# Kernel tuning notes

Hardware: AMD Instinct MI355X
Metric: run time of the kernel (lower is better)

The kernel has to match this reference:

```python
import jax, jax.numpy as jnp
import numpy as np

EPS = 1e-8  # matches torch F.cosine_similarity eps


def _normalize(x):
    n = jnp.sqrt(jnp.sum(x * x, axis=-1, keepdims=True))
    return x / jnp.maximum(n, EPS)


def _cross_entropy_diag(logits):
    # targets = arange(B): CE = mean(-log_softmax(logits)[i, i])
    logp = jax.nn.log_softmax(logits, axis=-1)
    return -jnp.mean(jnp.diagonal(logp))


def setup_inputs() -> dict:
    key = jax.random.key(0)
    k1, k2, k3 = jax.random.split(key, 3)
    B, D = 8192, 256
    return {
        "heavy_feat": jax.random.normal(k1, (B, D), dtype=jnp.float32),
        "light_feat": jax.random.normal(k2, (B, D), dtype=jnp.float32),
        "antigen_feat": jax.random.normal(k3, (B, D), dtype=jnp.float32),
    }


def reference(heavy_feat, light_feat, antigen_feat):
    h = _normalize(heavy_feat)   # [B, D]
    l = _normalize(light_feat)   # [B, D]
    a = _normalize(antigen_feat)  # [B, D]
    ha_sim = jnp.einsum("id,jd->ij", h, a)  # [B, B] cosine sims
    hl_sim = jnp.einsum("id,jd->ij", l, a)  # [B, B]
    return _cross_entropy_diag(ha_sim) + _cross_entropy_diag(hl_sim)
```

## Files before the change

### kernel.cpp

```cpp
#include <hip/hip_runtime.h>
#include <stdint.h>

#define BN_ 8192
#define DK_ 256
#define LOG2E 1.4426950408889634f
#define INVQ (1.0f / 16129.0f)
#define KQ   (LOG2E / 16129.0f)

typedef __attribute__((ext_vector_type(4))) float f32x4;
typedef __attribute__((ext_vector_type(4))) int i32x4;

#define GLD16(gp, lp)                                                   \
  __builtin_amdgcn_global_load_lds(                                     \
      (__attribute__((address_space(1))) void*)(gp),                    \
      (__attribute__((address_space(3))) void*)(lp), 16, 0, 0)

#define BAR() __builtin_amdgcn_s_barrier()
#define VM4() asm volatile("s_waitcnt vmcnt(4)" ::: "memory")
#define VM0() asm volatile("s_waitcnt vmcnt(0)" ::: "memory")

__global__ __launch_bounds__(256) void norm_kernel(
    const float* __restrict__ hf, const float* __restrict__ lf,
    const float* __restrict__ af, unsigned char* __restrict__ qbase,
    float* __restrict__ sumexp) {
  const int tid = threadIdx.x;
  if (blockIdx.x < 16) {
    f32x4 z = {0.f, 0.f, 0.f, 0.f};
    *(f32x4*)(sumexp + blockIdx.x * 1024 + tid * 4) = z;
  }
  const int w = tid >> 6, lane = tid & 63;
  const int grow = blockIdx.x * 4 + w;
  const int m = grow >> 13;
  const int r = grow & (BN_ - 1);
  const float* src = (m == 0) ? hf : (m == 1) ? lf : af;
  unsigned char* dst = qbase + (size_t)m * BN_ * DK_;
  const float4 v = ((const float4*)(src + (size_t)r * DK_))[lane];
  float ss = v.x * v.x + v.y * v.y + v.z * v.z + v.w * v.w;
#pragma unroll
  for (int mk = 32; mk >= 1; mk >>= 1) ss += __shfl_xor(ss, mk, 64);
  const float inv = 127.0f / fmaxf(sqrtf(ss), 1e-8f);
  const int q0 = (int)rintf(v.x * inv), q1 = (int)rintf(v.y * inv);
  const int q2 = (int)rintf(v.z * inv), q3 = (int)rintf(v.w * inv);
  const unsigned pk = (q0 & 255) | ((q1 & 255) << 8) | ((q2 & 255) << 16) |
                      ((unsigned)(q3 & 255) << 24);
  *(unsigned*)(dst + (size_t)r * DK_ + lane * 4) = pk;
}

__global__ __launch_bounds__(512, 2) void gemm_lse_kernel(
    const unsigned char* __restrict__ hl, const unsigned char* __restrict__ an,
    float* __restrict__ sumexp , float* __restrict__ diag ) {
  extern __shared__ char lds[];

  const int tid = threadIdx.x;
  const int lane = tid & 63, w = tid >> 6;
  const int wr = w >> 2, wc = w & 3;
  const int lmod = lane & 15, lhalf = lane >> 4;

  const int bid = blockIdx.x;
  const int swz = (bid & 7) * 32 + (bid >> 3);
  const int mt = swz >> 1;
  const int cg = swz & 1;

  const int aswz = 16 * ((tid & 15) ^ ((tid >> 4) & 15));
  const unsigned char* aG = hl + (size_t)(mt * 128 + (tid >> 4)) * DK_ + aswz;
  char* aD = lds + tid * 16;
  GLD16(aG, aD);
  GLD16(aG + 8192, aD + 8192);
  GLD16(aG + 16384, aD + 16384);
  GLD16(aG + 24576, aD + 24576);

  const int slog16 = 16 * ((lane & 3) ^ ((lane >> 3) & 3));
  const unsigned char* bB =
      an + (size_t)(cg * 4096 + wc * 64 + (lane >> 2)) * DK_ + slog16;
  char* ldsB = lds + 32768 + w * 8192 + lane * 16;

#define STAGEB(uu)                                                       \
  do {                                                                   \
    const int ct_ = (uu) >> 2, ku_ = (uu) & 3;                           \
    const unsigned char* g_ = bB + ct_ * 65536 + ku_ * 64;               \
    char* d_ = ldsB + ((uu) & 1) * 4096;                                 \
    GLD16(g_, d_);                                                       \
    GLD16(g_ + 4096, d_ + 1024);                                         \
    GLD16(g_ + 8192, d_ + 2048);                                         \
    GLD16(g_ + 12288, d_ + 3072);                                        \
  } while (0)

  STAGEB(0);
  VM4();
  BAR();

  i32x4 afr[4][4];
  {
    const char* aR = lds + (wr * 64 + lmod) * 256;
#pragma unroll
    for (int ku = 0; ku < 4; ++ku)
#pragma unroll
      for (int m = 0; m < 4; ++m)
        afr[ku][m] = *(const i32x4*)(aR + m * 4096 + 16 * ((ku * 4 + lhalf) ^ lmod));
  }

  const int rdoffB = lmod * 64 + 16 * (lhalf ^ ((lmod >> 1) & 3));
  const char* ldsBr = lds + 32768 + w * 8192;

  const int p = mt >> 6;
  const int D = (mt & 63) * 128 + wr * 64;
  const bool dWave = (wc == ((D >> 6) & 3)) && ((D >> 12) == cg);
  const int ctD = (D >> 8) & 15;

  float rsum[4][4];
#pragma unroll
  for (int m = 0; m < 4; ++m)
#pragma unroll
    for (int r = 0; r < 4; ++r) rsum[m][r] = 0.0f;

#pragma unroll 1
  for (int ct = 0; ct < 16; ++ct) {
    i32x4 acc[4][4];
#pragma unroll
    for (int m = 0; m < 4; ++m)
#pragma unroll
      for (int n = 0; n < 4; ++n) acc[m][n] = i32x4{0, 0, 0, 0};

#pragma unroll
    for (int ku = 0; ku < 4; ++ku) {
      const int u = ct * 4 + ku;
      if (u < 63) {
        STAGEB(u + 1);
        VM4();
      } else {
        VM0();
      }
      const char* Lb = ldsBr + (u & 1) * 4096;
      i32x4 bf[4];
#pragma unroll
      for (int n = 0; n < 4; ++n) bf[n] = *(const i32x4*)(Lb + n * 1024 + rdoffB);
#pragma unroll
      for (int m = 0; m < 4; ++m)
#pragma unroll
        for (int n = 0; n < 4; ++n)
          acc[m][n] = __builtin_amdgcn_mfma_i32_16x16x64_i8(afr[ku][m], bf[n], acc[m][n], 0, 0, 0);
    }

    if (dWave && ct == ctD) {
#pragma unroll
      for (int m = 0; m < 4; ++m)
#pragma unroll
        for (int r = 0; r < 4; ++r)
          if (lmod == lhalf * 4 + r)
            diag[p * BN_ + D + m * 16 + lmod] = (float)acc[m][m][r] * INVQ;
    }
#pragma unroll
    for (int m = 0; m < 4; ++m)
#pragma unroll
      for (int n = 0; n < 4; ++n)
#pragma unroll
        for (int r = 0; r < 4; ++r)
          rsum[m][r] += __builtin_amdgcn_exp2f((float)acc[m][n][r] * KQ);
  }

#pragma unroll
  for (int m = 0; m < 4; ++m)
#pragma unroll
    for (int r = 0; r < 4; ++r) {
      float v = rsum[m][r];
      v += __shfl_xor(v, 1, 64);
      v += __shfl_xor(v, 2, 64);
      v += __shfl_xor(v, 4, 64);
      v += __shfl_xor(v, 8, 64);
      if (lmod == 0)
        atomicAdd(&sumexp[p * BN_ + D + m * 16 + lhalf * 4 + r], v);
    }
#undef STAGEB
}

__global__ __launch_bounds__(1024) void finalize_kernel(
    const float* __restrict__ sumexp, const float* __restrict__ diag,
    float* __restrict__ out) {
  const int tid = threadIdx.x;
  float s = 0.0f;
  for (int i = tid; i < 2 * BN_; i += 1024) s += logf(sumexp[i]) - diag[i];
#pragma unroll
  for (int mk = 32; mk >= 1; mk >>= 1) s += __shfl_xor(s, mk, 64);
  __shared__ float red[16];
  if ((tid & 63) == 0) red[tid >> 6] = s;
  __syncthreads();
  if (tid == 0) {
    float t = 0.f;
#pragma unroll
    for (int j = 0; j < 16; ++j) t += red[j];
    out[0] = t * (1.0f / (float)BN_);
  }
}

extern "C" void kernel_launch(void* const* d_in, const int* in_sizes, int n_in,
                              void* d_out, int out_size, void* d_ws, size_t ws_size,
                              hipStream_t stream) {
  const float* hf = (const float*)d_in[0];
  const float* lf = (const float*)d_in[1];
  const float* af = (const float*)d_in[2];

  char* ws = (char*)d_ws;
  const size_t nmat = (size_t)BN_ * DK_;
  unsigned char* qbase = (unsigned char*)ws;
  unsigned char* hl = qbase;
  unsigned char* an = qbase + 2 * nmat;
  float* sumexp = (float*)(ws + 3 * nmat);
  float* diag = sumexp + 2 * BN_;

  hipFuncSetAttribute((const void*)gemm_lse_kernel,
                      hipFuncAttributeMaxDynamicSharedMemorySize, 98304);

  norm_kernel<<<(3 * BN_) / 4, 256, 0, stream>>>(hf, lf, af, qbase, sumexp);
  gemm_lse_kernel<<<256, 512, 98304, stream>>>(hl, an, sumexp, diag);
  finalize_kernel<<<1, 1024, 0, stream>>>(sumexp, diag, (float*)d_out);
}
```

Baseline: 65.09 us.

## Load B fragments directly from global memory and read A fragments from LDS per step

Drops the double-buffered global-to-LDS staging of the antigen (B) tiles and instead loads B fragments straight from global memory into registers in each k-step. A fragments are no longer kept in registers for the whole kernel but re-read from LDS each iteration, and LDS use falls from 96 KB to 32 KB. The aim is to cut register pressure, LDS traffic and the per-step waits and barriers, at the cost of uncoalesced, unpipelined global loads with latency that is exposed, unless occupancy and the L2 hide it.

After: 87.29 us. 1.34x slower.

```diff
diff --git a/kernel.cpp b/kernel.cpp
--- a/kernel.cpp
+++ b/kernel.cpp
@@ -16,7 +16,6 @@
       (__attribute__((address_space(3))) void*)(lp), 16, 0, 0)
 
 #define BAR() __builtin_amdgcn_s_barrier()
-#define VM4() asm volatile("s_waitcnt vmcnt(4)" ::: "memory")
 #define VM0() asm volatile("s_waitcnt vmcnt(0)" ::: "memory")
 
 __global__ __launch_bounds__(256) void norm_kernel(
@@ -68,39 +67,13 @@
   GLD16(aG + 8192, aD + 8192);
   GLD16(aG + 16384, aD + 16384);
   GLD16(aG + 24576, aD + 24576);
-
-  const int slog16 = 16 * ((lane & 3) ^ ((lane >> 3) & 3));
-  const unsigned char* bB =
-      an + (size_t)(cg * 4096 + wc * 64 + (lane >> 2)) * DK_ + slog16;
-  char* ldsB = lds + 32768 + w * 8192 + lane * 16;
-
-#define STAGEB(uu)                                                       \
-  do {                                                                   \
-    const int ct_ = (uu) >> 2, ku_ = (uu) & 3;                           \
-    const unsigned char* g_ = bB + ct_ * 65536 + ku_ * 64;               \
-    char* d_ = ldsB + ((uu) & 1) * 4096;                                 \
-    GLD16(g_, d_);                                                       \
-    GLD16(g_ + 4096, d_ + 1024);                                         \
-    GLD16(g_ + 8192, d_ + 2048);                                         \
-    GLD16(g_ + 12288, d_ + 3072);                                        \
-  } while (0)
-
-  STAGEB(0);
-  VM4();
+  VM0();
   BAR();
 
-  i32x4 afr[4][4];
-  {
-    const char* aR = lds + (wr * 64 + lmod) * 256;
-#pragma unroll
-    for (int ku = 0; ku < 4; ++ku)
-#pragma unroll
-      for (int m = 0; m < 4; ++m)
-        afr[ku][m] = *(const i32x4*)(aR + m * 4096 + 16 * ((ku * 4 + lhalf) ^ lmod));
-  }
+  const char* aR = lds + (wr * 64 + lmod) * 256;
 
-  const int rdoffB = lmod * 64 + 16 * (lhalf ^ ((lmod >> 1) & 3));
-  const char* ldsBr = lds + 32768 + w * 8192;
+  const unsigned char* bG =
+      an + (size_t)(cg * 4096 + wc * 64 + lmod) * DK_ + lhalf * 16;
 
   const int p = mt >> 6;
   const int D = (mt & 63) * 128 + wr * 64;
@@ -121,24 +94,21 @@
 #pragma unroll
       for (int n = 0; n < 4; ++n) acc[m][n] = i32x4{0, 0, 0, 0};
 
+    const unsigned char* bCt = bG + (size_t)ct * 65536;
 #pragma unroll
     for (int ku = 0; ku < 4; ++ku) {
-      const int u = ct * 4 + ku;
-      if (u < 63) {
-        STAGEB(u + 1);
-        VM4();
-      } else {
-        VM0();
-      }
-      const char* Lb = ldsBr + (u & 1) * 4096;
-      i32x4 bf[4];
+      i32x4 af[4], bf[4];
 #pragma unroll
-      for (int n = 0; n < 4; ++n) bf[n] = *(const i32x4*)(Lb + n * 1024 + rdoffB);
+      for (int n = 0; n < 4; ++n)
+        bf[n] = *(const i32x4*)(bCt + n * 4096 + ku * 64);
+#pragma unroll
+      for (int m = 0; m < 4; ++m)
+        af[m] = *(const i32x4*)(aR + m * 4096 + 16 * ((ku * 4 + lhalf) ^ lmod));
 #pragma unroll
       for (int m = 0; m < 4; ++m)
 #pragma unroll
         for (int n = 0; n < 4; ++n)
-          acc[m][n] = __builtin_amdgcn_mfma_i32_16x16x64_i8(afr[ku][m], bf[n], acc[m][n], 0, 0, 0);
+          acc[m][n] = __builtin_amdgcn_mfma_i32_16x16x64_i8(af[m], bf[n], acc[m][n], 0, 0, 0);
     }
 
     if (dWave && ct == ctD) {
@@ -170,7 +140,6 @@
       if (lmod == 0)
         atomicAdd(&sumexp[p * BN_ + D + m * 16 + lhalf * 4 + r], v);
     }
-#undef STAGEB
 }
 
 __global__ __launch_bounds__(1024) void finalize_kernel(
@@ -208,9 +177,9 @@
   float* diag = sumexp + 2 * BN_;
 
   hipFuncSetAttribute((const void*)gemm_lse_kernel,
-                      hipFuncAttributeMaxDynamicSharedMemorySize, 98304);
+                      hipFuncAttributeMaxDynamicSharedMemorySize, 32768);
 
   norm_kernel<<<(3 * BN_) / 4, 256, 0, stream>>>(hf, lf, af, qbase, sumexp);
-  gemm_lse_kernel<<<256, 512, 98304, stream>>>(hl, an, sumexp, diag);
+  gemm_lse_kernel<<<256, 512, 32768, stream>>>(hl, an, sumexp, diag);
   finalize_kernel<<<1, 1024, 0, stream>>>(sumexp, diag, (float*)d_out);
 }
```
